# Performance work log

Measured on AMD Instinct MI355X. Metric: run time of the kernel, lower is better.

Reference implementation:

```python
import jax, jax.numpy as jnp
import numpy as np

MD = 4       # max displacement per level (md=[4,...] in VCN)
WSIZE = 3    # truncation window half-size in flow_reg


def _corrf(ref, tar, md=MD):
    """VCN.corrf: per-channel shifted-product 4D cost volume + leaky_relu.
    cost[b,c,i,j,y,x] = leaky_relu(ref[b,c,y,x] * tar[b,c,y+(j-md), x+(i-md)], 0.1)
    (zero outside valid region, matching the torch zero-filled buffer)."""
    B, C, H, W = ref.shape
    U = 2 * md + 1
    tar_pad = jnp.pad(tar, ((0, 0), (0, 0), (md, md), (md, md)))
    # dim 2 ordered as i*U + j (i = x-shift index, j = y-shift index)
    shifts = jnp.stack([tar_pad[:, :, j:j + H, i:i + W]
                        for i in range(U) for j in range(U)], axis=2)
    cost = jax.nn.leaky_relu(ref[:, :, None] * shifts, 0.1)
    return cost.reshape(B, C, U, U, H, W)


def _flow_reg(x, md=MD, wsize=WSIZE):
    """flow_reg with ent=True: argmax -> 7x7 box mask over (u,v) (the MaxPool3d on a
    one-hot scatter is exactly a Chebyshev-box around the argmax) -> masked softmax
    over u*v -> soft-argmax flow + local/global entropies."""
    B, U, V, H, W = x.shape
    idx = jnp.argmax(x.reshape(B, U * V, H, W), axis=1)         # (B,H,W)
    ub, vb = idx // V, idx % V
    uu = jnp.arange(U)[None, :, None, None, None]
    vv = jnp.arange(V)[None, None, :, None, None]
    mask = (jnp.abs(uu - ub[:, None, None]) <= wsize) & \
           (jnp.abs(vv - vb[:, None, None]) <= wsize)           # (B,U,V,H,W)
    neg_inf = jnp.array(-jnp.inf, x.dtype)
    p = jax.nn.softmax(jnp.where(mask, x, neg_inf).reshape(B, U * V, H, W),
                       axis=1).reshape(B, U, V, H, W)
    fx = (jnp.arange(U) - md).astype(x.dtype)[None, :, None, None, None]
    fy = (jnp.arange(V) - md).astype(x.dtype)[None, None, :, None, None]
    outx = jnp.sum(p * fx, axis=(1, 2))[:, None]                # (B,1,H,W)
    outy = jnp.sum(p * fy, axis=(1, 2))[:, None]
    def _ent(q):
        return (-q * jnp.log(jnp.clip(q, 1e-9, 1 - 1e-9))).sum(axis=(1, 2))[:, None]
    local_ent = _ent(p) / np.log((2 * wsize + 1) ** 2).astype(np.float32)
    pg = jax.nn.softmax(x.reshape(B, U * V, H, W), axis=1).reshape(B, U, V, H, W)
    global_ent = _ent(pg) / np.log(U * V).astype(np.float32)
    return jnp.concatenate([outx, outy], 1), jnp.concatenate([local_ent, global_ent], 1)


def _warp(x, flo):
    """grid_sample-based backward warp (bilinear, zero padding, align_corners=True)
    plus the in-bounds mask, exactly as VCN's warp()."""
    B, C, H, W = x.shape
    px = jnp.arange(W, dtype=flo.dtype)[None, None, :] + flo[:, 0]   # (B,H,W)
    py = jnp.arange(H, dtype=flo.dtype)[None, :, None] + flo[:, 1]
    inb = (jnp.abs(2.0 * px / max(W - 1, 1) - 1.0) < 1) & \
          (jnp.abs(2.0 * py / max(H - 1, 1) - 1.0) < 1)
    x0 = jnp.floor(px); y0 = jnp.floor(py)
    wx = px - x0; wy = py - y0
    x0i = x0.astype(jnp.int32); y0i = y0.astype(jnp.int32)
    flat = x.reshape(B, C, H * W)
    def tap(yi, xi, wgt):
        valid = (xi >= 0) & (xi < W) & (yi >= 0) & (yi < H)
        lin = jnp.clip(yi, 0, H - 1) * W + jnp.clip(xi, 0, W - 1)
        v = jax.vmap(lambda img, l: img[:, l])(flat, lin)            # (B,C,H,W)
        return v * (wgt * valid.astype(x.dtype))[:, None]
    out = (tap(y0i,     x0i,     (1 - wx) * (1 - wy)) +
           tap(y0i,     x0i + 1, wx * (1 - wy)) +
           tap(y0i + 1, x0i,     (1 - wx) * wy) +
           tap(y0i + 1, x0i + 1, wx * wy))
    return out * inb.astype(x.dtype)[:, None], inb


def setup_inputs() -> dict:
    key = jax.random.key(0)
    k1, k2, k3 = jax.random.split(key, 3)
    B, C, H, W, F = 2, 128, 64, 64, 16
    ref = jax.random.normal(k1, (B, C, H, W), jnp.float32) * 0.5
    tar = jax.random.normal(k2, (B, C, H, W), jnp.float32) * 0.5
    pw = jax.random.normal(k3, (F, C), jnp.float32) / np.sqrt(C).astype(np.float32)
    return {"ref_feat": ref, "tar_feat": tar, "proj_w": pw}


def reference(ref_feat, tar_feat, proj_w):
    B, C, H, W = ref_feat.shape
    F_ = proj_w.shape[0]
    U = 2 * MD + 1
    cost = _corrf(ref_feat, tar_feat)                       # (B,C,U,U,H,W)
    # 1x1 channel contraction of the 4D cost volume (butterfly4D input proj)
    cvol = jnp.einsum('bcuvhw,fc->bfuvhw', cost, proj_w)    # (B,F,U,U,H,W)
    flow_h, ent_h = _flow_reg(cvol.reshape(B * F_, U, U, H, W))
    flow = flow_h.reshape(B, F_, 2, H, W)[:, 0]             # first hypothesis
    warped, _ = _warp(tar_feat, flow)
    return jnp.concatenate([flow_h, ent_h], axis=1), warped
```

## Files before the change

### kernel.cpp

```cpp
#include <hip/hip_runtime.h>
#include <math.h>

#define B_ 2
#define C_ 128
#define H_ 64
#define W_ 64
#define F_ 16
#define U_ 9
#define MD_ 4
#define HW_ (H_*W_)
#define BF_ (B_*F_)

typedef float f32x4 __attribute__((ext_vector_type(4)));
typedef float f32x2 __attribute__((ext_vector_type(2)));
typedef _Float16 f16x2 __attribute__((ext_vector_type(2)));
typedef _Float16 f16x4 __attribute__((ext_vector_type(4)));
typedef _Float16 f16x8 __attribute__((ext_vector_type(8)));

#define XSCALE   64.0f
#define WSCALE   256.0f
#define UNSCALE  (1.0f / 16384.0f)

#define TB0  0
#define TB1  7344
#define TSTR 34
#define REFO 14688
#define SM_  5832
#define SI_  6344
#define SU_  6856
#define FX_  9928
#define FY_  9944
#define LDSZ 16800

static __device__ __forceinline__ f16x8 cat4(f16x2 a, f16x2 b, f16x2 c, f16x2 d) {
    f16x4 ab = __builtin_shufflevector(a, b, 0, 1, 2, 3);
    f16x4 cd = __builtin_shufflevector(c, d, 0, 1, 2, 3);
    return __builtin_shufflevector(ab, cd, 0, 1, 2, 3, 4, 5, 6, 7);
}

static __device__ __forceinline__ void split2(f32x2 p, f16x2& hi, f16x2& lo) {
    hi = __builtin_bit_cast(f16x2, __builtin_amdgcn_cvt_pkrtz(p.x, p.y));
    f32x2 hf; hf.x = (float)hi.x; hf.y = (float)hi.y;
    f32x2 l = p - hf;
    lo = __builtin_bit_cast(f16x2, __builtin_amdgcn_cvt_pkrtz(l.x, l.y));
}

__global__ __launch_bounds__(512, 2)
void fused_kernel(const float* __restrict__ ref,
                  const float* __restrict__ tar,
                  const float* __restrict__ pw,
                  float* __restrict__ out0,
                  float* __restrict__ warped) {
    const int t    = threadIdx.x;
    const int lane = t & 63;
    const int wid  = t >> 6;
    const int ml   = lane & 15;
    const int grp  = lane >> 4;

    const int n0 = blockIdx.x;
    const int L  = (n0 & 7) * 64 + (n0 >> 3);
    const int b  = L >> 8;
    const int y  = (L >> 2) & 63;
    const int x0 = (L & 3) * 16;

    const int start = wid ? (1 + wid * 10) : 0;

    __shared__ float lds[LDSZ];

    const float* refB = ref + ((size_t)b * C_) * HW_ + y * W_ + x0;
    const float* tarB = tar + ((size_t)b * C_) * HW_;

    int uA[11], vA[11];
    #pragma unroll
    for (int i = 0; i < 11; ++i) {
        int uv = start + i;
        int uu = uv / 9;
        uA[i] = uu; vA[i] = uv - uu * 9;
    }

    #pragma unroll
    for (int it = 0; it < 4; ++it) {
        int idx = it * 512 + t;
        int c = idx >> 4, px = idx & 15;
        lds[REFO + px * 132 + c] = refB[(size_t)c * HW_ + px] * XSCALE;
    }

    const int seg   = t >> 1;
    const int chalf = (t & 1) * 16;
    const bool sactive = (seg < 216);
    const int sr   = seg / 24;
    const int scol = seg - sr * 24;
    const int ysr  = y + sr - 4;
    const int xg   = x0 - 4 + scol;
    const bool sok = sactive && ((unsigned)ysr < 64u) && ((unsigned)xg < 64u);
    const int ysc  = ysr < 0 ? 0 : (ysr > 63 ? 63 : ysr);
    const int xgc  = xg  < 0 ? 0 : (xg  > 63 ? 63 : xg);
    const float* tS = tarB + (size_t)chalf * HW_ + ysc * W_ + xgc;

    auto STAGE = [&](int kcv, int bufbase, bool zfill) {
        if (sok) {
            float* dst = lds + bufbase + seg * TSTR + chalf;
            const float* g = tS + (size_t)(kcv * 32) * HW_;
            #pragma unroll
            for (int c0 = 0; c0 < 16; ++c0) dst[c0] = g[(size_t)c0 * HW_];
        } else if (sactive && zfill) {
            float* dst = lds + bufbase + seg * TSTR + chalf;
            #pragma unroll
            for (int c0 = 0; c0 < 16; ++c0) dst[c0] = 0.f;
        }
    };

    f32x4 acc[11];
    #pragma unroll
    for (int i = 0; i < 11; ++i) acc[i] = f32x4{0.f, 0.f, 0.f, 0.f};

    STAGE(0, TB0, true);
    __syncthreads();

    #pragma unroll
    for (int kc = 0; kc < 4; ++kc) {
        const int tb = (kc & 1) ? TB1 : TB0;
        if (kc == 0) STAGE(1, TB1, true);
        else if (kc == 1) STAGE(2, TB0, false);
        else if (kc == 2) STAGE(3, TB1, false);

        f32x4 wa = *(const f32x4*)(pw + ml * C_ + kc * 32 + grp * 8);
        f32x4 wb = *(const f32x4*)(pw + ml * C_ + kc * 32 + grp * 8 + 4);
        f16x2 wh[4], wl[4];
        {
            f32x2 p;
            p.x = wa.x * WSCALE; p.y = wa.y * WSCALE; split2(p, wh[0], wl[0]);
            p.x = wa.z * WSCALE; p.y = wa.w * WSCALE; split2(p, wh[1], wl[1]);
            p.x = wb.x * WSCALE; p.y = wb.y * WSCALE; split2(p, wh[2], wl[2]);
            p.x = wb.z * WSCALE; p.y = wb.w * WSCALE; split2(p, wh[3], wl[3]);
        }
        f16x8 whi = cat4(wh[0], wh[1], wh[2], wh[3]);
        f16x8 wlo = cat4(wl[0], wl[1], wl[2], wl[3]);

        f32x4 rva = *(const f32x4*)(lds + REFO + ml * 132 + kc * 32 + grp * 8);
        f32x4 rvb = *(const f32x4*)(lds + REFO + ml * 132 + kc * 32 + grp * 8 + 4);
        f32x2 rv2[4];
        rv2[0].x = rva.x; rv2[0].y = rva.y;
        rv2[1].x = rva.z; rv2[1].y = rva.w;
        rv2[2].x = rvb.x; rv2[2].y = rvb.y;
        rv2[3].x = rvb.z; rv2[3].y = rvb.w;

#define UVBODY(i) {                                                           \
        const int cb = tb + (vA[i] * 24 + ml + uA[i]) * TSTR + grp * 8;       \
        f16x2 xh4[4], xl4[4];                                                 \
        _Pragma("unroll")                                                     \
        for (int jp = 0; jp < 4; ++jp) {                                      \
            f32x2 tj = *(const f32x2*)(lds + cb + 2 * jp);                    \
            f32x2 p  = rv2[jp] * tj;                                          \
            f32x2 p1 = p * 0.1f;                                              \
            p = __builtin_elementwise_max(p, p1);                             \
            split2(p, xh4[jp], xl4[jp]);                                      \
        }                                                                     \
        f16x8 xhi = cat4(xh4[0], xh4[1], xh4[2], xh4[3]);                     \
        f16x8 xlo = cat4(xl4[0], xl4[1], xl4[2], xl4[3]);                     \
        acc[i] = __builtin_amdgcn_mfma_f32_16x16x32_f16(whi, xhi, acc[i], 0, 0, 0); \
        acc[i] = __builtin_amdgcn_mfma_f32_16x16x32_f16(wlo, xhi, acc[i], 0, 0, 0); \
        acc[i] = __builtin_amdgcn_mfma_f32_16x16x32_f16(whi, xlo, acc[i], 0, 0, 0); }

        #pragma unroll
        for (int i = 0; i < 10; ++i) UVBODY(i);
        if (wid == 0) UVBODY(10);

        __syncthreads();
    }

    const int rem = t & 63;
    const int fl  = rem >> 4;
    const int px  = rem & 15;

    for (int P = 0; P < 4; ++P) {
#define BOUNCE(i) {                                                           \
        if (grp == P) {                                                       \
            int ba = (start + (i)) * 18 + ml;                                 \
            lds[ba        ] = acc[i][0] * UNSCALE;                            \
            lds[ba + 1458 ] = acc[i][1] * UNSCALE;                            \
            lds[ba + 2916 ] = acc[i][2] * UNSCALE;                            \
            lds[ba + 4374 ] = acc[i][3] * UNSCALE; } }
        #pragma unroll
        for (int i = 0; i < 10; ++i) BOUNCE(i);
        if (wid == 0) BOUNCE(10);
        __syncthreads();

        float vv[11];
        #pragma unroll
        for (int i = 0; i < 10; ++i)
            vv[i] = lds[fl * 1458 + (start + i) * 18 + px];
        if (wid == 0) vv[10] = lds[fl * 1458 + 10 * 18 + px];
        float mv = vv[0]; int bi = start;
        #pragma unroll
        for (int i = 1; i < 10; ++i)
            if (vv[i] > mv) { mv = vv[i]; bi = start + i; }
        if (wid == 0 && vv[10] > mv) { mv = vv[10]; bi = 10; }
        lds[SM_ + t] = mv; lds[SI_ + t] = (float)bi;
        __syncthreads();

        float m = lds[SM_ + rem]; int best = (int)lds[SI_ + rem];
        #pragma unroll
        for (int k = 1; k < 8; ++k) {
            float mk = lds[SM_ + k * 64 + rem];
            if (mk > m) { m = mk; best = (int)lds[SI_ + k * 64 + rem]; }
        }
        int ub = best / 9, vb = best - 9 * (best / 9);

        float S = 0.f, A = 0.f, Sx = 0.f, Sy = 0.f, gS = 0.f, gA = 0.f;
#define PH2B(i) {                                                             \
        float d = vv[i] - m; float z = __expf(d);                             \
        gS += z; gA = fmaf(z, d, gA);                                         \
        int duc = uA[i] - ub, dvc = vA[i] - vb;                               \
        bool msk = (duc <= 3) && (duc >= -3) && (dvc <= 3) && (dvc >= -3);    \
        float zm = msk ? z : 0.f, dm = msk ? d : 0.f;                         \
        S += zm; A = fmaf(zm, dm, A);                                         \
        Sx = fmaf(zm, (float)(uA[i] - MD_), Sx);                              \
        Sy = fmaf(zm, (float)(vA[i] - MD_), Sy); }
        #pragma unroll
        for (int i = 0; i < 10; ++i) PH2B(i);
        if (wid == 0) PH2B(10);

        lds[SU_ + 0 * 512 + t] = S;  lds[SU_ + 1 * 512 + t] = A;
        lds[SU_ + 2 * 512 + t] = Sx; lds[SU_ + 3 * 512 + t] = Sy;
        lds[SU_ + 4 * 512 + t] = gS; lds[SU_ + 5 * 512 + t] = gA;
        __syncthreads();

        if (t < 64) {
            float rq[6];
            #pragma unroll
            for (int q = 0; q < 6; ++q) {
                float s = lds[SU_ + q * 512 + t];
                #pragma unroll
                for (int k = 1; k < 8; ++k) s += lds[SU_ + q * 512 + k * 64 + t];
                rq[q] = s;
            }
            float invS = 1.f / rq[0];
            float outx = rq[2] * invS;
            float outy = rq[3] * invS;
            float lent = (logf(rq[0]) - rq[1] * invS) * (1.0f / logf(49.0f));
            float gent = (logf(rq[4]) - rq[5] / rq[4]) * (1.0f / logf(81.0f));
            float* op = out0 + ((size_t)(b * F_ + P * 4 + (t >> 4)) * 4) * HW_
                      + y * W_ + x0 + (t & 15);
            op[0 * HW_] = outx;
            op[1 * HW_] = outy;
            op[2 * HW_] = lent;
            op[3 * HW_] = gent;
            if (P == 0 && t < 16) { lds[FX_ + t] = outx; lds[FY_ + t] = outy; }
        }
    }

    {
        const int pxi = t & 15;
        const int xw  = x0 + pxi;
        float fx = lds[FX_ + pxi], fy = lds[FY_ + pxi];
        float pxw = (float)xw + fx;
        float pyw = (float)y  + fy;
        bool inb = (fabsf(2.0f * pxw / 63.0f - 1.0f) < 1.0f) &&
                   (fabsf(2.0f * pyw / 63.0f - 1.0f) < 1.0f);
        float xf = floorf(pxw), yf = floorf(pyw);
        float wx = pxw - xf, wy = pyw - yf;
        int x0i = (int)xf, y0i = (int)yf;
        auto off = [&](int yi, int xi, float wgt, float& mw) -> int {
            bool v = ((unsigned)xi < (unsigned)W_) && ((unsigned)yi < (unsigned)H_);
            int xc = xi < 0 ? 0 : (xi > W_ - 1 ? W_ - 1 : xi);
            int yc = yi < 0 ? 0 : (yi > H_ - 1 ? H_ - 1 : yi);
            mw = v ? wgt : 0.f;
            return yc * W_ + xc;
        };
        float m00, m01, m10, m11;
        int o00 = off(y0i,     x0i,     (1.f - wx) * (1.f - wy), m00);
        int o01 = off(y0i,     x0i + 1, wx * (1.f - wy),         m01);
        int o10 = off(y0i + 1, x0i,     (1.f - wx) * wy,         m10);
        int o11 = off(y0i + 1, x0i + 1, wx * wy,                 m11);
        #pragma unroll
        for (int it = 0; it < 4; ++it) {
            int c = (t >> 4) + 32 * it;
            const float* img = tarB + (size_t)c * HW_;
            float a = img[o00] * m00 + img[o01] * m01
                    + img[o10] * m10 + img[o11] * m11;
            warped[((size_t)(b * C_ + c)) * HW_ + y * W_ + xw] = inb ? a : 0.f;
        }
    }
}

extern "C" void kernel_launch(void* const* d_in, const int* in_sizes, int n_in,
                              void* d_out, int out_size, void* d_ws, size_t ws_size,
                              hipStream_t stream) {
    const float* ref = (const float*)d_in[0];
    const float* tar = (const float*)d_in[1];
    const float* pw  = (const float*)d_in[2];
    float* out0 = (float*)d_out;
    float* out1 = out0 + (size_t)BF_ * 4 * HW_;
    (void)d_ws; (void)ws_size;

    fused_kernel<<<512, 512, 0, stream>>>(ref, tar, pw, out0, out1);
}
```

Before: 106.6 us.

## Read target features directly from global memory instead of LDS double-buffer staging

Removes the double-buffered LDS staging of the shifted target tile and its per-chunk barriers. Each lane now gathers its 8 target channels straight from global memory, with precomputed clamped offsets, a column mask and a row-validity skip. This shrinks LDS use and drops the syncs, but issues many strided, uncoalesced global loads that depend on the cache to absorb the reuse across the 81 shifts.

```diff
diff --git a/kernel.cpp b/kernel.cpp
--- a/kernel.cpp
+++ b/kernel.cpp
@@ -21,16 +21,13 @@
 #define WSCALE   256.0f
 #define UNSCALE  (1.0f / 16384.0f)
 
-#define TB0  0
-#define TB1  7344
-#define TSTR 34
-#define REFO 14688
 #define SM_  5832
 #define SI_  6344
 #define SU_  6856
 #define FX_  9928
 #define FY_  9944
-#define LDSZ 16800
+#define REFO 10000
+#define LDSZ 12112
 
 static __device__ __forceinline__ f16x8 cat4(f16x2 a, f16x2 b, f16x2 c, f16x2 d) {
     f16x4 ab = __builtin_shufflevector(a, b, 0, 1, 2, 3);
@@ -70,12 +67,21 @@
     const float* refB = ref + ((size_t)b * C_) * HW_ + y * W_ + x0;
     const float* tarB = tar + ((size_t)b * C_) * HW_;
 
-    int uA[11], vA[11];
+    int uA[11], vA[11], voff[11];
+    float mf[11];
+    bool rok[11];
     #pragma unroll
     for (int i = 0; i < 11; ++i) {
         int uv = start + i;
         int uu = uv / 9;
         uA[i] = uu; vA[i] = uv - uu * 9;
+        int ysr = y + vA[i] - 4;
+        rok[i] = ((unsigned)ysr < 64u);
+        int xc  = x0 + ml + uA[i] - 4;
+        mf[i]   = ((unsigned)xc < 64u) ? 1.f : 0.f;
+        int xcl = xc  < 0 ? 0 : (xc  > 63 ? 63 : xc);
+        int ycl = ysr < 0 ? 0 : (ysr > 63 ? 63 : ysr);
+        voff[i] = grp * 8 * HW_ + ycl * W_ + xcl;
     }
 
     #pragma unroll
@@ -84,46 +90,14 @@
         int c = idx >> 4, px = idx & 15;
         lds[REFO + px * 132 + c] = refB[(size_t)c * HW_ + px] * XSCALE;
     }
-
-    const int seg   = t >> 1;
-    const int chalf = (t & 1) * 16;
-    const bool sactive = (seg < 216);
-    const int sr   = seg / 24;
-    const int scol = seg - sr * 24;
-    const int ysr  = y + sr - 4;
-    const int xg   = x0 - 4 + scol;
-    const bool sok = sactive && ((unsigned)ysr < 64u) && ((unsigned)xg < 64u);
-    const int ysc  = ysr < 0 ? 0 : (ysr > 63 ? 63 : ysr);
-    const int xgc  = xg  < 0 ? 0 : (xg  > 63 ? 63 : xg);
-    const float* tS = tarB + (size_t)chalf * HW_ + ysc * W_ + xgc;
-
-    auto STAGE = [&](int kcv, int bufbase, bool zfill) {
-        if (sok) {
-            float* dst = lds + bufbase + seg * TSTR + chalf;
-            const float* g = tS + (size_t)(kcv * 32) * HW_;
-            #pragma unroll
-            for (int c0 = 0; c0 < 16; ++c0) dst[c0] = g[(size_t)c0 * HW_];
-        } else if (sactive && zfill) {
-            float* dst = lds + bufbase + seg * TSTR + chalf;
-            #pragma unroll
-            for (int c0 = 0; c0 < 16; ++c0) dst[c0] = 0.f;
-        }
-    };
+    __syncthreads();
 
     f32x4 acc[11];
     #pragma unroll
     for (int i = 0; i < 11; ++i) acc[i] = f32x4{0.f, 0.f, 0.f, 0.f};
 
-    STAGE(0, TB0, true);
-    __syncthreads();
-
     #pragma unroll
     for (int kc = 0; kc < 4; ++kc) {
-        const int tb = (kc & 1) ? TB1 : TB0;
-        if (kc == 0) STAGE(1, TB1, true);
-        else if (kc == 1) STAGE(2, TB0, false);
-        else if (kc == 2) STAGE(3, TB1, false);
-
         f32x4 wa = *(const f32x4*)(pw + ml * C_ + kc * 32 + grp * 8);
         f32x4 wb = *(const f32x4*)(pw + ml * C_ + kc * 32 + grp * 8 + 4);
         f16x2 wh[4], wl[4];
@@ -145,13 +119,20 @@
         rv2[2].x = rvb.x; rv2[2].y = rvb.y;
         rv2[3].x = rvb.z; rv2[3].y = rvb.w;
 
-#define UVBODY(i) {                                                           \
-        const int cb = tb + (vA[i] * 24 + ml + uA[i]) * TSTR + grp * 8;       \
+        const float* pk = tarB + (size_t)(kc * 32) * HW_;
+
+#define UVBODY(i) if (rok[i]) {                                               \
+        float tv[8];                                                          \
+        _Pragma("unroll")                                                     \
+        for (int c8 = 0; c8 < 8; ++c8)                                        \
+            tv[c8] = pk[(size_t)c8 * HW_ + voff[i]];                          \
+        f32x2 mp; mp.x = mf[i]; mp.y = mf[i];                                 \
         f16x2 xh4[4], xl4[4];                                                 \
         _Pragma("unroll")                                                     \
         for (int jp = 0; jp < 4; ++jp) {                                      \
-            f32x2 tj = *(const f32x2*)(lds + cb + 2 * jp);                    \
+            f32x2 tj; tj.x = tv[2 * jp]; tj.y = tv[2 * jp + 1];               \
             f32x2 p  = rv2[jp] * tj;                                          \
+            p = p * mp;                                                       \
             f32x2 p1 = p * 0.1f;                                              \
             p = __builtin_elementwise_max(p, p1);                             \
             split2(p, xh4[jp], xl4[jp]);                                      \
@@ -165,8 +146,6 @@
         #pragma unroll
         for (int i = 0; i < 10; ++i) UVBODY(i);
         if (wid == 0) UVBODY(10);
-
-        __syncthreads();
     }
 
     const int rem = t & 63;
```

After: 116.7 us. +9.5%, slower.

## Vectorize tar staging, prefetch into registers, and double-buffer LDS tap reads

Applied to the files above, without the earlier changes.

Staging of the target window changes from scalar per-channel loads to 16-byte vector loads along x (one thread per channel and row, 288 active threads). Each load is realigned with a compile-time shift and an edge mask before it is written to LDS. The global loads for the next channel chunk are issued into registers before the MFMA loop and written to LDS after it, so their latency overlaps compute. The LDS tap reads inside the uv loop are software-pipelined one iteration ahead, and offsets are precomputed. The cost is higher register pressure from the 6-vector prefetch and the double tap buffer under launch_bounds(512,2), which could cause spills.

```diff
diff --git a/kernel.cpp b/kernel.cpp
--- a/kernel.cpp
+++ b/kernel.cpp
@@ -61,7 +61,8 @@
     const int L  = (n0 & 7) * 64 + (n0 >> 3);
     const int b  = L >> 8;
     const int y  = (L >> 2) & 63;
-    const int x0 = (L & 3) * 16;
+    const int xq = L & 3;
+    const int x0 = xq * 16;
 
     const int start = wid ? (1 + wid * 10) : 0;
 
@@ -70,59 +71,89 @@
     const float* refB = ref + ((size_t)b * C_) * HW_ + y * W_ + x0;
     const float* tarB = tar + ((size_t)b * C_) * HW_;
 
-    int uA[11], vA[11];
+    int off[11];
     #pragma unroll
     for (int i = 0; i < 11; ++i) {
         int uv = start + i;
         int uu = uv / 9;
-        uA[i] = uu; vA[i] = uv - uu * 9;
-    }
-
+        off[i] = ((uv - uu * 9) * 24 + uu) * TSTR;
+    }
+    const int mlg = ml * TSTR + grp * 8;
+
+    const int sc = t & 31;
+    const int sr = t >> 5;
+    const bool sact = (t < 288);
+    const int ysr  = y + sr - 4;
+    const bool sok = sact && ((unsigned)ysr < 64u);
+    const int xlo = (xq == 0) ? 0 : (xq == 3 ? 40 : x0 - 4);
+    const int sh  = x0 - 4 - xlo;
+    const float* tS = tarB + (size_t)sc * HW_ + (sok ? ysr : 0) * W_ + xlo;
+    unsigned cmask = 0;
+    #pragma unroll
+    for (int j = 0; j < 24; ++j)
+        if ((unsigned)(x0 - 4 + j) < 64u) cmask |= (1u << j);
+
+    f32x4 g[6];
+#define ISSUE(KC) if (sok) {                                                  \
+        const float* gp = tS + (size_t)((KC) * 32) * HW_;                     \
+        _Pragma("unroll")                                                     \
+        for (int q = 0; q < 6; ++q) g[q] = *(const f32x4*)(gp + 4 * q);       \
+    }
+
+#define SWR(BUF, S) {                                                         \
+        float* dst = lds + (BUF) + (sr * 24) * TSTR + sc;                     \
+        _Pragma("unroll")                                                     \
+        for (int j = 0; j < 24; ++j) {                                        \
+            float v_ = 0.f;                                                   \
+            if ((j + (S)) >= 0 && (j + (S)) < 24)                             \
+                if ((cmask >> j) & 1u) v_ = g[(j + (S)) >> 2][(j + (S)) & 3]; \
+            dst[j * TSTR] = v_;                                               \
+        } }
+
+#define SWRITE(KC, BUF) {                                                     \
+        if (sok) {                                                            \
+            if (sh == 0)     { SWR(BUF, 0) }                                  \
+            else if (sh < 0) { SWR(BUF, -4) }                                 \
+            else             { SWR(BUF, 4) }                                  \
+        } else if (sact && (KC) < 2) {     \
+            float* dst = lds + (BUF) + (sr * 24) * TSTR + sc;                 \
+            _Pragma("unroll")                                                 \
+            for (int j = 0; j < 24; ++j) dst[j * TSTR] = 0.f;                 \
+        } }
+
+#define TCOMP(SL, I) {                                                        \
+        f16x2 xh4[4], xl4[4];                                                 \
+        _Pragma("unroll")                                                     \
+        for (int jp = 0; jp < 4; ++jp) {                                      \
+            f32x2 p  = rv2[jp] * tv[SL][jp];                                  \
+            f32x2 p1 = p * 0.1f;                                              \
+            p = __builtin_elementwise_max(p, p1);                             \
+            split2(p, xh4[jp], xl4[jp]);                                      \
+        }                                                                     \
+        f16x8 xhi = cat4(xh4[0], xh4[1], xh4[2], xh4[3]);                     \
+        f16x8 xlo = cat4(xl4[0], xl4[1], xl4[2], xl4[3]);                     \
+        acc[I] = __builtin_amdgcn_mfma_f32_16x16x32_f16(whi, xhi, acc[I], 0, 0, 0); \
+        acc[I] = __builtin_amdgcn_mfma_f32_16x16x32_f16(wlo, xhi, acc[I], 0, 0, 0); \
+        acc[I] = __builtin_amdgcn_mfma_f32_16x16x32_f16(whi, xlo, acc[I], 0, 0, 0); }
+
+    f32x4 acc[11];
+    #pragma unroll
+    for (int i = 0; i < 11; ++i) acc[i] = f32x4{0.f, 0.f, 0.f, 0.f};
+
+    ISSUE(0);
     #pragma unroll
     for (int it = 0; it < 4; ++it) {
         int idx = it * 512 + t;
         int c = idx >> 4, px = idx & 15;
         lds[REFO + px * 132 + c] = refB[(size_t)c * HW_ + px] * XSCALE;
     }
-
-    const int seg   = t >> 1;
-    const int chalf = (t & 1) * 16;
-    const bool sactive = (seg < 216);
-    const int sr   = seg / 24;
-    const int scol = seg - sr * 24;
-    const int ysr  = y + sr - 4;
-    const int xg   = x0 - 4 + scol;
-    const bool sok = sactive && ((unsigned)ysr < 64u) && ((unsigned)xg < 64u);
-    const int ysc  = ysr < 0 ? 0 : (ysr > 63 ? 63 : ysr);
-    const int xgc  = xg  < 0 ? 0 : (xg  > 63 ? 63 : xg);
-    const float* tS = tarB + (size_t)chalf * HW_ + ysc * W_ + xgc;
-
-    auto STAGE = [&](int kcv, int bufbase, bool zfill) {
-        if (sok) {
-            float* dst = lds + bufbase + seg * TSTR + chalf;
-            const float* g = tS + (size_t)(kcv * 32) * HW_;
-            #pragma unroll
-            for (int c0 = 0; c0 < 16; ++c0) dst[c0] = g[(size_t)c0 * HW_];
-        } else if (sactive && zfill) {
-            float* dst = lds + bufbase + seg * TSTR + chalf;
-            #pragma unroll
-            for (int c0 = 0; c0 < 16; ++c0) dst[c0] = 0.f;
-        }
-    };
-
-    f32x4 acc[11];
-    #pragma unroll
-    for (int i = 0; i < 11; ++i) acc[i] = f32x4{0.f, 0.f, 0.f, 0.f};
-
-    STAGE(0, TB0, true);
+    SWRITE(0, TB0);
+    ISSUE(1);
     __syncthreads();
 
     #pragma unroll
     for (int kc = 0; kc < 4; ++kc) {
         const int tb = (kc & 1) ? TB1 : TB0;
-        if (kc == 0) STAGE(1, TB1, true);
-        else if (kc == 1) STAGE(2, TB0, false);
-        else if (kc == 2) STAGE(3, TB1, false);
 
         f32x4 wa = *(const f32x4*)(pw + ml * C_ + kc * 32 + grp * 8);
         f32x4 wb = *(const f32x4*)(pw + ml * C_ + kc * 32 + grp * 8 + 4);
@@ -145,30 +176,35 @@
         rv2[2].x = rvb.x; rv2[2].y = rvb.y;
         rv2[3].x = rvb.z; rv2[3].y = rvb.w;
 
-#define UVBODY(i) {                                                           \
-        const int cb = tb + (vA[i] * 24 + ml + uA[i]) * TSTR + grp * 8;       \
-        f16x2 xh4[4], xl4[4];                                                 \
-        _Pragma("unroll")                                                     \
-        for (int jp = 0; jp < 4; ++jp) {                                      \
-            f32x2 tj = *(const f32x2*)(lds + cb + 2 * jp);                    \
-            f32x2 p  = rv2[jp] * tj;                                          \
-            f32x2 p1 = p * 0.1f;                                              \
-            p = __builtin_elementwise_max(p, p1);                             \
-            split2(p, xh4[jp], xl4[jp]);                                      \
-        }                                                                     \
-        f16x8 xhi = cat4(xh4[0], xh4[1], xh4[2], xh4[3]);                     \
-        f16x8 xlo = cat4(xl4[0], xl4[1], xl4[2], xl4[3]);                     \
-        acc[i] = __builtin_amdgcn_mfma_f32_16x16x32_f16(whi, xhi, acc[i], 0, 0, 0); \
-        acc[i] = __builtin_amdgcn_mfma_f32_16x16x32_f16(wlo, xhi, acc[i], 0, 0, 0); \
-        acc[i] = __builtin_amdgcn_mfma_f32_16x16x32_f16(whi, xlo, acc[i], 0, 0, 0); }
-
-        #pragma unroll
-        for (int i = 0; i < 10; ++i) UVBODY(i);
-        if (wid == 0) UVBODY(10);
-
+        f32x2 tv[2][4];
+        {
+            const float* tp = lds + tb + off[0] + mlg;
+            tv[0][0] = *(const f32x2*)(tp);     tv[0][1] = *(const f32x2*)(tp + 2);
+            tv[0][2] = *(const f32x2*)(tp + 4); tv[0][3] = *(const f32x2*)(tp + 6);
+        }
+        #pragma unroll
+        for (int i = 0; i < 10; ++i) {
+            const int nx = (i + 1) & 1, cu = i & 1;
+            const float* tp = lds + tb + off[i + 1] + mlg;
+            tv[nx][0] = *(const f32x2*)(tp);     tv[nx][1] = *(const f32x2*)(tp + 2);
+            tv[nx][2] = *(const f32x2*)(tp + 4); tv[nx][3] = *(const f32x2*)(tp + 6);
+            TCOMP(cu, i);
+        }
+        if (wid == 0) TCOMP(0, 10);
+
+        if (kc == 0) { SWRITE(1, TB1); ISSUE(2); }
+        else if (kc == 1) { SWRITE(2, TB0); ISSUE(3); }
+        else if (kc == 2) { SWRITE(3, TB1); }
         __syncthreads();
     }
 
+    int uA[11], vA[11];
+    #pragma unroll
+    for (int i = 0; i < 11; ++i) {
+        int uv = start + i;
+        int uu = uv / 9;
+        uA[i] = uu; vA[i] = uv - uu * 9;
+    }
     const int rem = t & 63;
     const int fl  = rem >> 4;
     const int px  = rem & 15;
@@ -261,7 +297,7 @@
         float xf = floorf(pxw), yf = floorf(pyw);
         float wx = pxw - xf, wy = pyw - yf;
         int x0i = (int)xf, y0i = (int)yf;
-        auto off = [&](int yi, int xi, float wgt, float& mw) -> int {
+        auto offn = [&](int yi, int xi, float wgt, float& mw) -> int {
             bool v = ((unsigned)xi < (unsigned)W_) && ((unsigned)yi < (unsigned)H_);
             int xc = xi < 0 ? 0 : (xi > W_ - 1 ? W_ - 1 : xi);
             int yc = yi < 0 ? 0 : (yi > H_ - 1 ? H_ - 1 : yi);
@@ -269,10 +305,10 @@
             return yc * W_ + xc;
         };
         float m00, m01, m10, m11;
-        int o00 = off(y0i,     x0i,     (1.f - wx) * (1.f - wy), m00);
-        int o01 = off(y0i,     x0i + 1, wx * (1.f - wy),         m01);
-        int o10 = off(y0i + 1, x0i,     (1.f - wx) * wy,         m10);
-        int o11 = off(y0i + 1, x0i + 1, wx * wy,                 m11);
+        int o00 = offn(y0i,     x0i,     (1.f - wx) * (1.f - wy), m00);
+        int o01 = offn(y0i,     x0i + 1, wx * (1.f - wy),         m01);
+        int o10 = offn(y0i + 1, x0i,     (1.f - wx) * wy,         m10);
+        int o11 = offn(y0i + 1, x0i + 1, wx * wy,                 m11);
         #pragma unroll
         for (int it = 0; it < 4; ++it) {
             int c = (t >> 4) + 32 * it;
```

Measured after the change: 108.2 us. Within noise of the previous version (+1.5%).

## Use 12 waves per block and reduce flow_reg directly from MFMA accumulators

Applied to the files above, without the earlier changes.

Blocks grow from 8 to 12 waves, and the 81 displacement slots are redistributed as 7 or 6 per wave instead of 10 or 11. This cuts per-wave MFMA work and accumulator registers. The old four-pass LDS bounce of accumulators is replaced by a single pass: each wave computes argmax and softmax partial sums straight from its accumulator registers for all four rows, then three cross-wave LDS reductions combine them. This removes many barriers and LDS round trips, at the cost of larger blocks, more LDS traffic per reduction round, and possible occupancy limits under launch_bounds(768,2).

```diff
diff --git a/kernel.cpp b/kernel.cpp
--- a/kernel.cpp
+++ b/kernel.cpp
@@ -25,11 +25,11 @@
 #define TB1  7344
 #define TSTR 34
 #define REFO 14688
-#define SM_  5832
-#define SI_  6344
-#define SU_  6856
-#define FX_  9928
-#define FY_  9944
+#define MXo  0
+#define IXo  3168
+#define SBo  6336
+#define FX_  12672
+#define FY_  12688
 #define LDSZ 16800
 
 static __device__ __forceinline__ f16x8 cat4(f16x2 a, f16x2 b, f16x2 c, f16x2 d) {
@@ -45,7 +45,7 @@
     lo = __builtin_bit_cast(f16x2, __builtin_amdgcn_cvt_pkrtz(l.x, l.y));
 }
 
-__global__ __launch_bounds__(512, 2)
+__global__ __launch_bounds__(768, 2)
 void fused_kernel(const float* __restrict__ ref,
                   const float* __restrict__ tar,
                   const float* __restrict__ pw,
@@ -63,36 +63,33 @@
     const int y  = (L >> 2) & 63;
     const int x0 = (L & 3) * 16;
 
-    const int start = wid ? (1 + wid * 10) : 0;
+    const bool big = (wid < 9);
+    const int start = __builtin_amdgcn_readfirstlane(
+        big ? wid * 7 : 63 + (wid - 9) * 6);
 
     __shared__ float lds[LDSZ];
 
     const float* refB = ref + ((size_t)b * C_) * HW_ + y * W_ + x0;
     const float* tarB = tar + ((size_t)b * C_) * HW_;
 
-    int uA[11], vA[11];
-    #pragma unroll
-    for (int i = 0; i < 11; ++i) {
+    int off[7], uA[7], vA[7];
+    #pragma unroll
+    for (int i = 0; i < 7; ++i) {
         int uv = start + i;
         int uu = uv / 9;
         uA[i] = uu; vA[i] = uv - uu * 9;
-    }
-
-    #pragma unroll
-    for (int it = 0; it < 4; ++it) {
-        int idx = it * 512 + t;
-        int c = idx >> 4, px = idx & 15;
-        lds[REFO + px * 132 + c] = refB[(size_t)c * HW_ + px] * XSCALE;
-    }
+        off[i] = (vA[i] * 24 + uu) * TSTR;
+    }
+    const int mlg = ml * TSTR + grp * 8;
 
     const int seg   = t >> 1;
     const int chalf = (t & 1) * 16;
-    const bool sactive = (seg < 216);
+    const bool sact = (seg < 216);
     const int sr   = seg / 24;
     const int scol = seg - sr * 24;
     const int ysr  = y + sr - 4;
     const int xg   = x0 - 4 + scol;
-    const bool sok = sactive && ((unsigned)ysr < 64u) && ((unsigned)xg < 64u);
+    const bool sok = sact && ((unsigned)ysr < 64u) && ((unsigned)xg < 64u);
     const int ysc  = ysr < 0 ? 0 : (ysr > 63 ? 63 : ysr);
     const int xgc  = xg  < 0 ? 0 : (xg  > 63 ? 63 : xg);
     const float* tS = tarB + (size_t)chalf * HW_ + ysc * W_ + xgc;
@@ -103,17 +100,25 @@
             const float* g = tS + (size_t)(kcv * 32) * HW_;
             #pragma unroll
             for (int c0 = 0; c0 < 16; ++c0) dst[c0] = g[(size_t)c0 * HW_];
-        } else if (sactive && zfill) {
+        } else if (sact && zfill) {
             float* dst = lds + bufbase + seg * TSTR + chalf;
             #pragma unroll
             for (int c0 = 0; c0 < 16; ++c0) dst[c0] = 0.f;
         }
     };
 
-    f32x4 acc[11];
-    #pragma unroll
-    for (int i = 0; i < 11; ++i) acc[i] = f32x4{0.f, 0.f, 0.f, 0.f};
-
+    f32x4 acc[7];
+    #pragma unroll
+    for (int i = 0; i < 7; ++i) acc[i] = f32x4{0.f, 0.f, 0.f, 0.f};
+
+    #pragma unroll
+    for (int it = 0; it < 3; ++it) {
+        int idx = it * 768 + t;
+        if (idx < 2048) {
+            int c = idx >> 4, px = idx & 15;
+            lds[REFO + px * 132 + c] = refB[(size_t)c * HW_ + px] * XSCALE;
+        }
+    }
     STAGE(0, TB0, true);
     __syncthreads();
 
@@ -146,11 +151,11 @@
         rv2[3].x = rvb.z; rv2[3].y = rvb.w;
 
 #define UVBODY(i) {                                                           \
-        const int cb = tb + (vA[i] * 24 + ml + uA[i]) * TSTR + grp * 8;       \
+        const float* tp = lds + tb + off[i] + mlg;                            \
         f16x2 xh4[4], xl4[4];                                                 \
         _Pragma("unroll")                                                     \
         for (int jp = 0; jp < 4; ++jp) {                                      \
-            f32x2 tj = *(const f32x2*)(lds + cb + 2 * jp);                    \
+            f32x2 tj = *(const f32x2*)(tp + 2 * jp);                          \
             f32x2 p  = rv2[jp] * tj;                                          \
             f32x2 p1 = p * 0.1f;                                              \
             p = __builtin_elementwise_max(p, p1);                             \
@@ -163,94 +168,112 @@
         acc[i] = __builtin_amdgcn_mfma_f32_16x16x32_f16(whi, xlo, acc[i], 0, 0, 0); }
 
         #pragma unroll
-        for (int i = 0; i < 10; ++i) UVBODY(i);
-        if (wid == 0) UVBODY(10);
+        for (int i = 0; i < 6; ++i) UVBODY(i);
+        if (big) UVBODY(6);
 
         __syncthreads();
     }
 
-    const int rem = t & 63;
-    const int fl  = rem >> 4;
-    const int px  = rem & 15;
-
-    for (int P = 0; P < 4; ++P) {
-#define BOUNCE(i) {                                                           \
-        if (grp == P) {                                                       \
-            int ba = (start + (i)) * 18 + ml;                                 \
-            lds[ba        ] = acc[i][0] * UNSCALE;                            \
-            lds[ba + 1458 ] = acc[i][1] * UNSCALE;                            \
-            lds[ba + 2916 ] = acc[i][2] * UNSCALE;                            \
-            lds[ba + 4374 ] = acc[i][3] * UNSCALE; } }
-        #pragma unroll
-        for (int i = 0; i < 10; ++i) BOUNCE(i);
-        if (wid == 0) BOUNCE(10);
-        __syncthreads();
-
-        float vv[11];
-        #pragma unroll
-        for (int i = 0; i < 10; ++i)
-            vv[i] = lds[fl * 1458 + (start + i) * 18 + px];
-        if (wid == 0) vv[10] = lds[fl * 1458 + 10 * 18 + px];
-        float mv = vv[0]; int bi = start;
-        #pragma unroll
-        for (int i = 1; i < 10; ++i)
-            if (vv[i] > mv) { mv = vv[i]; bi = start + i; }
-        if (wid == 0 && vv[10] > mv) { mv = vv[10]; bi = 10; }
-        lds[SM_ + t] = mv; lds[SI_ + t] = (float)bi;
-        __syncthreads();
-
-        float m = lds[SM_ + rem]; int best = (int)lds[SI_ + rem];
-        #pragma unroll
-        for (int k = 1; k < 8; ++k) {
-            float mk = lds[SM_ + k * 64 + rem];
-            if (mk > m) { m = mk; best = (int)lds[SI_ + k * 64 + rem]; }
-        }
-        int ub = best / 9, vb = best - 9 * (best / 9);
-
-        float S = 0.f, A = 0.f, Sx = 0.f, Sy = 0.f, gS = 0.f, gA = 0.f;
-#define PH2B(i) {                                                             \
-        float d = vv[i] - m; float z = __expf(d);                             \
-        gS += z; gA = fmaf(z, d, gA);                                         \
-        int duc = uA[i] - ub, dvc = vA[i] - vb;                               \
-        bool msk = (duc <= 3) && (duc >= -3) && (dvc <= 3) && (dvc >= -3);    \
-        float zm = msk ? z : 0.f, dm = msk ? d : 0.f;                         \
-        S += zm; A = fmaf(zm, dm, A);                                         \
-        Sx = fmaf(zm, (float)(uA[i] - MD_), Sx);                              \
-        Sy = fmaf(zm, (float)(vA[i] - MD_), Sy); }
-        #pragma unroll
-        for (int i = 0; i < 10; ++i) PH2B(i);
-        if (wid == 0) PH2B(10);
-
-        lds[SU_ + 0 * 512 + t] = S;  lds[SU_ + 1 * 512 + t] = A;
-        lds[SU_ + 2 * 512 + t] = Sx; lds[SU_ + 3 * 512 + t] = Sy;
-        lds[SU_ + 4 * 512 + t] = gS; lds[SU_ + 5 * 512 + t] = gA;
-        __syncthreads();
-
-        if (t < 64) {
-            float rq[6];
-            #pragma unroll
-            for (int q = 0; q < 6; ++q) {
-                float s = lds[SU_ + q * 512 + t];
-                #pragma unroll
-                for (int k = 1; k < 8; ++k) s += lds[SU_ + q * 512 + k * 64 + t];
-                rq[q] = s;
-            }
-            float invS = 1.f / rq[0];
-            float outx = rq[2] * invS;
-            float outy = rq[3] * invS;
-            float lent = (logf(rq[0]) - rq[1] * invS) * (1.0f / logf(49.0f));
-            float gent = (logf(rq[4]) - rq[5] / rq[4]) * (1.0f / logf(81.0f));
-            float* op = out0 + ((size_t)(b * F_ + P * 4 + (t >> 4)) * 4) * HW_
-                      + y * W_ + x0 + (t & 15);
+    #pragma unroll
+    for (int i = 0; i < 7; ++i) acc[i] = acc[i] * UNSCALE;
+
+    f32x4 mx = acc[0];
+    f32x4 bix = f32x4{(float)start, (float)start, (float)start, (float)start};
+    #pragma unroll
+    for (int i = 1; i < 6; ++i)
+        #pragma unroll
+        for (int r = 0; r < 4; ++r)
+            if (acc[i][r] > mx[r]) { mx[r] = acc[i][r]; bix[r] = (float)(start + i); }
+    if (big) {
+        #pragma unroll
+        for (int r = 0; r < 4; ++r)
+            if (acc[6][r] > mx[r]) { mx[r] = acc[6][r]; bix[r] = (float)(start + 6); }
+    }
+    *(f32x4*)(lds + MXo + (wid * 4 + grp) * 66 + ml * 4) = mx;
+    *(f32x4*)(lds + IXo + (wid * 4 + grp) * 66 + ml * 4) = bix;
+    __syncthreads();
+
+    f32x4 gm = *(const f32x4*)(lds + MXo + grp * 66 + ml * 4);
+    f32x4 gb = *(const f32x4*)(lds + IXo + grp * 66 + ml * 4);
+    #pragma unroll
+    for (int ch = 1; ch < 12; ++ch) {
+        f32x4 cm = *(const f32x4*)(lds + MXo + (ch * 4 + grp) * 66 + ml * 4);
+        f32x4 cb = *(const f32x4*)(lds + IXo + (ch * 4 + grp) * 66 + ml * 4);
+        #pragma unroll
+        for (int r = 0; r < 4; ++r)
+            if (cm[r] > gm[r]) { gm[r] = cm[r]; gb[r] = cb[r]; }
+    }
+    int ub[4], vb[4];
+    #pragma unroll
+    for (int r = 0; r < 4; ++r) {
+        int bI = (int)gb[r];
+        ub[r] = bI / 9; vb[r] = bI - 9 * ub[r];
+    }
+
+    float S[4]  = {0.f,0.f,0.f,0.f}, Aa[4] = {0.f,0.f,0.f,0.f};
+    float Sx[4] = {0.f,0.f,0.f,0.f}, Sy[4] = {0.f,0.f,0.f,0.f};
+    float gS[4] = {0.f,0.f,0.f,0.f}, gA[4] = {0.f,0.f,0.f,0.f};
+#define PHB(i) {                                                              \
+        _Pragma("unroll")                                                     \
+        for (int r = 0; r < 4; ++r) {                                         \
+            float d = acc[i][r] - gm[r];                                      \
+            float z = __expf(d);                                              \
+            gS[r] += z; gA[r] = fmaf(z, d, gA[r]);                            \
+            int duc = uA[i] - ub[r], dvc = vA[i] - vb[r];                     \
+            bool msk = (duc <= 3) && (duc >= -3) && (dvc <= 3) && (dvc >= -3);\
+            float zm = msk ? z : 0.f, dm = msk ? d : 0.f;                     \
+            S[r] += zm; Aa[r] = fmaf(zm, dm, Aa[r]);                          \
+            Sx[r] = fmaf(zm, (float)(uA[i] - MD_), Sx[r]);                    \
+            Sy[r] = fmaf(zm, (float)(vA[i] - MD_), Sy[r]);                    \
+        } }
+    #pragma unroll
+    for (int i = 0; i < 6; ++i) PHB(i);
+    if (big) PHB(6);
+
+    float rq[6];
+    const int cml = t & 15, cgrp = (t >> 4) & 3;
+#define ROUND(QA, QB, RA, RB) {                                               \
+        *(f32x4*)(lds + SBo + ((0 * 12 + wid) * 4 + grp) * 66 + ml * 4) =     \
+            f32x4{QA[0], QA[1], QA[2], QA[3]};                                \
+        *(f32x4*)(lds + SBo + ((1 * 12 + wid) * 4 + grp) * 66 + ml * 4) =     \
+            f32x4{QB[0], QB[1], QB[2], QB[3]};                                \
+        __syncthreads();                                                      \
+        if (t < 64) {                                                         \
+            f32x4 sa = *(const f32x4*)(lds + SBo + ((0) * 4 + cgrp) * 66 + cml * 4); \
+            f32x4 sb = *(const f32x4*)(lds + SBo + ((12) * 4 + cgrp) * 66 + cml * 4); \
+            _Pragma("unroll")                                                 \
+            for (int ch = 1; ch < 12; ++ch) {                                 \
+                sa += *(const f32x4*)(lds + SBo + ((ch) * 4 + cgrp) * 66 + cml * 4);      \
+                sb += *(const f32x4*)(lds + SBo + ((12 + ch) * 4 + cgrp) * 66 + cml * 4); \
+            }                                                                 \
+            RA = sa; RB = sb;                                                 \
+        }                                                                     \
+        __syncthreads(); }
+    f32x4 r0v, r1v, r2v, r3v, r4v, r5v;
+    ROUND(S,  Aa, r0v, r1v)
+    ROUND(Sx, Sy, r2v, r3v)
+    ROUND(gS, gA, r4v, r5v)
+
+    if (t < 64) {
+        #pragma unroll
+        for (int r = 0; r < 4; ++r) {
+            float invS = 1.f / r0v[r];
+            float outx = r2v[r] * invS;
+            float outy = r3v[r] * invS;
+            float lent = (logf(r0v[r]) - r1v[r] * invS) * (1.0f / logf(49.0f));
+            float gent = (logf(r4v[r]) - r5v[r] / r4v[r]) * (1.0f / logf(81.0f));
+            float* op = out0 + ((size_t)(b * F_ + cgrp * 4 + r) * 4) * HW_
+                      + y * W_ + x0 + cml;
             op[0 * HW_] = outx;
             op[1 * HW_] = outy;
             op[2 * HW_] = lent;
             op[3 * HW_] = gent;
-            if (P == 0 && t < 16) { lds[FX_ + t] = outx; lds[FY_ + t] = outy; }
-        }
-    }
-
-    {
+            if (r == 0 && cgrp == 0) { lds[FX_ + cml] = outx; lds[FY_ + cml] = outy; }
+        }
+    }
+    __syncthreads();
+
+    if (t < 512) {
         const int pxi = t & 15;
         const int xw  = x0 + pxi;
         float fx = lds[FX_ + pxi], fy = lds[FY_ + pxi];
@@ -261,7 +284,7 @@
         float xf = floorf(pxw), yf = floorf(pyw);
         float wx = pxw - xf, wy = pyw - yf;
         int x0i = (int)xf, y0i = (int)yf;
-        auto off = [&](int yi, int xi, float wgt, float& mw) -> int {
+        auto offn = [&](int yi, int xi, float wgt, float& mw) -> int {
             bool v = ((unsigned)xi < (unsigned)W_) && ((unsigned)yi < (unsigned)H_);
             int xc = xi < 0 ? 0 : (xi > W_ - 1 ? W_ - 1 : xi);
             int yc = yi < 0 ? 0 : (yi > H_ - 1 ? H_ - 1 : yi);
@@ -269,10 +292,10 @@
             return yc * W_ + xc;
         };
         float m00, m01, m10, m11;
-        int o00 = off(y0i,     x0i,     (1.f - wx) * (1.f - wy), m00);
-        int o01 = off(y0i,     x0i + 1, wx * (1.f - wy),         m01);
-        int o10 = off(y0i + 1, x0i,     (1.f - wx) * wy,         m10);
-        int o11 = off(y0i + 1, x0i + 1, wx * wy,                 m11);
+        int o00 = offn(y0i,     x0i,     (1.f - wx) * (1.f - wy), m00);
+        int o01 = offn(y0i,     x0i + 1, wx * (1.f - wy),         m01);
+        int o10 = offn(y0i + 1, x0i,     (1.f - wx) * wy,         m10);
+        int o11 = offn(y0i + 1, x0i + 1, wx * wy,                 m11);
         #pragma unroll
         for (int it = 0; it < 4; ++it) {
             int c = (t >> 4) + 32 * it;
@@ -294,5 +317,5 @@
     float* out1 = out0 + (size_t)BF_ * 4 * HW_;
     (void)d_ws; (void)ws_size;
 
-    fused_kernel<<<512, 512, 0, stream>>>(ref, tar, pw, out0, out1);
+    fused_kernel<<<512, 768, 0, stream>>>(ref, tar, pw, out0, out1);
 }
```

Result: no change. 104.5 us (-2.0%).
